# Kernel tuning notes

Measured on AMD Instinct MI355X. Metric: run time of the kernel, lower is better.

## Reference

```python
import jax, jax.numpy as jnp
import numpy as np

D = 1024   # embedding_dim
H = 16     # head_num
DH = D // H
STD = 0.02


def setup_inputs() -> dict:
    key = jax.random.key(0)
    ks = jax.random.split(key, 8)
    B, S = 16, 2048
    inp = {
        "hidden_states": jax.random.normal(ks[0], (B, S, D), dtype=jnp.float32),
        "attention_mask": jnp.zeros((B, 1, S), dtype=jnp.float32),
        # nn.Linear params, stored as [in, out] for direct matmul
        "Wq": jax.random.normal(ks[1], (D, D), dtype=jnp.float32) * STD,
        "bq": jnp.zeros((D,), dtype=jnp.float32),
        "Wqa": jax.random.normal(ks[2], (D, H), dtype=jnp.float32) * STD,
        "bqa": jnp.zeros((H,), dtype=jnp.float32),
        "Wk": jax.random.normal(ks[3], (D, D), dtype=jnp.float32) * STD,
        "bk": jnp.zeros((D,), dtype=jnp.float32),
        "Wka": jax.random.normal(ks[4], (D, H), dtype=jnp.float32) * STD,
        "bka": jnp.zeros((H,), dtype=jnp.float32),
        "Wt": jax.random.normal(ks[5], (D, D), dtype=jnp.float32) * STD,
        "bt": jnp.zeros((D,), dtype=jnp.float32),
    }
    return inp


def reference(hidden_states, attention_mask, Wq, bq, Wqa, bqa, Wk, bk, Wka, bka, Wt, bt):
    B, S, _ = hidden_states.shape
    scale = 1.0 / np.sqrt(DH).astype(np.float32)

    mixed_q = hidden_states @ Wq + bq          # [B,S,D]
    mixed_k = hidden_states @ Wk + bk          # [B,S,D]

    # per-head query pooling scores: [B,S,H] -> [B,H,S]
    q_score = jnp.transpose(mixed_q @ Wqa + bqa, (0, 2, 1)) * scale + attention_mask
    q_weight = jax.nn.softmax(q_score, axis=-1)                 # [B,H,S]

    q_layer = mixed_q.reshape(B, S, H, DH).transpose(0, 2, 1, 3)  # [B,H,S,dh]
    pooled_q = jnp.einsum('bhs,bhsd->bhd', q_weight, q_layer)     # [B,H,dh]
    pooled_q_flat = pooled_q.reshape(B, 1, D)                     # [B,1,D] (head-major)

    # elementwise modulate keys with pooled query (broadcast, no repeat)
    mixed_qk = mixed_k * pooled_q_flat                            # [B,S,D]

    qk_score = jnp.transpose(mixed_qk @ Wka + bka, (0, 2, 1)) * scale + attention_mask
    qk_weight = jax.nn.softmax(qk_score, axis=-1)                 # [B,H,S]

    k_layer = mixed_qk.reshape(B, S, H, DH).transpose(0, 2, 1, 3)  # [B,H,S,dh]
    pooled_k = jnp.einsum('bhs,bhsd->bhd', qk_weight, k_layer)     # [B,H,dh]

    weighted = pooled_k[:, :, None, :] * q_layer                   # [B,H,S,dh]
    weighted = weighted.transpose(0, 2, 1, 3).reshape(B, S, D)     # [B,S,D]

    return weighted @ Wt + bt + mixed_q
```

## Files before the change

kernel.cpp:

```cpp
#include <hip/hip_runtime.h>
#include <hip/hip_bf16.h>
#include <stdint.h>

#define D_ 1024
#define H_ 16
#define DH_ 64
#define S_ 2048
#define B_ 16
static constexpr float SCALE = 0.125f;

typedef __bf16 bf16_t;
typedef __bf16 bf16x8 __attribute__((ext_vector_type(8)));
typedef __bf16 bf16x4 __attribute__((ext_vector_type(4)));
typedef float  f32x4  __attribute__((ext_vector_type(4)));

__device__ __forceinline__ void llds16(const void* g, void* l) {
  __builtin_amdgcn_global_load_lds(
      (const __attribute__((address_space(1))) void*)g,
      (__attribute__((address_space(3))) void*)l, 16, 0, 0);
}

__global__ __launch_bounds__(256)
void f32_to_bf16(const float* __restrict__ src, bf16_t* __restrict__ dst) {
  size_t base = ((size_t)blockIdx.x * 256 + threadIdx.x) * 8;
  f32x4 a = *(const f32x4*)&src[base];
  f32x4 b = *(const f32x4*)&src[base + 4];
  bf16x8 o;
#pragma unroll
  for (int i = 0; i < 4; ++i) { o[i] = (bf16_t)a[i]; o[4 + i] = (bf16_t)b[i]; }
  *(bf16x8*)&dst[base] = o;
}

__global__ __launch_bounds__(256)
void transpose1024(const float* __restrict__ src, bf16_t* __restrict__ dst) {
  __shared__ bf16_t t[64][65];
  const int n0 = blockIdx.x * 64, k0 = blockIdx.y * 64;
  const int r = threadIdx.x >> 4, c4 = (threadIdx.x & 15) * 4;
#pragma unroll
  for (int p = 0; p < 4; ++p) {
    int row = p * 16 + r;
    f32x4 f = *(const f32x4*)&src[(size_t)(k0 + row) * 1024 + n0 + c4];
#pragma unroll
    for (int i = 0; i < 4; ++i) t[row][c4 + i] = (bf16_t)f[i];
  }
  __syncthreads();
#pragma unroll
  for (int p = 0; p < 4; ++p) {
    int row = p * 16 + r;
    bf16x4 v;
#pragma unroll
    for (int i = 0; i < 4; ++i) v[i] = t[c4 + i][row];
    *(bf16x4*)&dst[(size_t)(n0 + row) * 1024 + k0 + c4] = v;
  }
}

__global__ __launch_bounds__(256)
void transpose_small(const float* __restrict__ src, bf16_t* __restrict__ dst) {
  int k = blockIdx.x * 256 + threadIdx.x;
  if (k < 1024) {
#pragma unroll
    for (int h = 0; h < H_; ++h) dst[h * 1024 + k] = (bf16_t)src[k * H_ + h];
  }
}

__global__ __launch_bounds__(256)
void conv_misc(const float* bqa, const float* bka, const float* mask,
               bf16_t* obqa, bf16_t* obka, bf16_t* omask) {
  int i = blockIdx.x * 256 + threadIdx.x;
  const float* src; bf16_t* dst; int off;
  if      (i < 16)    { src = bqa;  dst = obqa;  off = i; }
  else if (i < 32)    { src = bka;  dst = obka;  off = i - 16; }
  else if (i < 32800) { src = mask; dst = omask; off = i - 32; }
  else return;
  dst[off] = (bf16_t)src[off];
}

template <int MODE>
__global__ __launch_bounds__(512, 1)
void gemm256(const bf16_t* __restrict__ A, const bf16_t* __restrict__ BT,
             const float* __restrict__ bias, void* __restrict__ Cout,
             const float* __restrict__ pscale, const bf16_t* __restrict__ resid) {
  constexpr int K = 1024;
  __shared__ __align__(16) bf16_t lds[2][2][256 * 64];
  const int tid = threadIdx.x;
  const int lane = tid & 63, wid = tid >> 6;
  const int wm = wid >> 2, wn = wid & 3;

  const int wgid = (blockIdx.x & 7) * 64 + (blockIdx.x >> 3);
  const int m0 = (wgid >> 2) * 256;
  const int n0 = (wgid & 3) * 256;

  const bf16_t* gA[4];
  const bf16_t* gB[4];
  int ldsOff[4];
#pragma unroll
  for (int i = 0; i < 4; ++i) {
    int c = i * 512 + tid;
    int r = c >> 3, j = c & 7;
    int col = ((j ^ (r & 7)) << 3);
    gA[i] = A  + (size_t)(m0 + r) * K + col;
    gB[i] = BT + (size_t)(n0 + r) * K + col;
    ldsOff[i] = c * 8;
  }

  f32x4 acc[8][4] = {};
  const int ar = lane & 15;
  const int kq = lane >> 4;

  bf16_t* curA = &lds[0][0][0]; bf16_t* curB = &lds[0][1][0];
  bf16_t* nxtA = &lds[1][0][0]; bf16_t* nxtB = &lds[1][1][0];

#pragma unroll
  for (int i = 0; i < 4; ++i) { llds16(gA[i], curA + ldsOff[i]); llds16(gB[i], curB + ldsOff[i]); }

  for (int t = 0; t < 16; ++t) {
    if (t < 15) {
      const int koff = (t + 1) * 64;
#pragma unroll
      for (int i = 0; i < 4; ++i) {
        llds16(gA[i] + koff, nxtA + ldsOff[i]);
        llds16(gB[i] + koff, nxtB + ldsOff[i]);
      }
      asm volatile("s_waitcnt vmcnt(8)" ::: "memory");
    } else {
      asm volatile("s_waitcnt vmcnt(0)" ::: "memory");
    }
    __builtin_amdgcn_s_barrier();

#pragma unroll
    for (int h = 0; h < 2; ++h) {
      bf16x8 af[8], bg[4];
#pragma unroll
      for (int m = 0; m < 8; ++m) {
        int r = wm * 128 + m * 16 + ar;
        af[m] = *(const bf16x8*)&curA[r * 64 + (((h * 4 + kq) ^ (r & 7)) << 3)];
      }
#pragma unroll
      for (int n = 0; n < 4; ++n) {
        int r = wn * 64 + n * 16 + ar;
        bg[n] = *(const bf16x8*)&curB[r * 64 + (((h * 4 + kq) ^ (r & 7)) << 3)];
      }
      __builtin_amdgcn_s_setprio(1);
#pragma unroll
      for (int m = 0; m < 8; ++m)
#pragma unroll
        for (int n = 0; n < 4; ++n)
          acc[m][n] = __builtin_amdgcn_mfma_f32_16x16x32_bf16(af[m], bg[n], acc[m][n], 0, 0, 0);
      __builtin_amdgcn_s_setprio(0);
    }
    __builtin_amdgcn_s_barrier();
    bf16_t* tA = curA; curA = nxtA; nxtA = tA;
    bf16_t* tB = curB; curB = nxtB; nxtB = tB;
  }

  float* st = (float*)(&lds[0][0][0]) + wid * (16 * 68);
  const int b = m0 / S_;
  const int erow = lane >> 2;
  const int ecol = (lane & 3) * 16;
  const int gcb = n0 + wn * 64;
  const int qrow = (lane >> 4) * 4;
  const int qcol = lane & 15;
  f32x4 bb[4], ps[4];
#pragma unroll
  for (int q = 0; q < 4; ++q) bb[q] = *(const f32x4*)&bias[gcb + ecol + q * 4];
  if (MODE == 1) {
#pragma unroll
    for (int q = 0; q < 4; ++q) ps[q] = *(const f32x4*)&pscale[b * D_ + gcb + ecol + q * 4];
  }
#pragma unroll
  for (int m = 0; m < 8; ++m) {
#pragma unroll
    for (int n = 0; n < 4; ++n)
#pragma unroll
      for (int j = 0; j < 4; ++j)
        st[(qrow + j) * 68 + n * 16 + qcol] = acc[m][n][j];
    asm volatile("s_waitcnt lgkmcnt(0)" ::: "memory");
    __builtin_amdgcn_sched_barrier(0);
    const int grow = m0 + wm * 128 + m * 16 + erow;
    f32x4 v[4];
#pragma unroll
    for (int q = 0; q < 4; ++q) v[q] = *(f32x4*)&st[erow * 68 + ecol + q * 4];
#pragma unroll
    for (int q = 0; q < 4; ++q)
#pragma unroll
      for (int i = 0; i < 4; ++i) v[q][i] += bb[q][i];
    if (MODE == 1) {
#pragma unroll
      for (int q = 0; q < 4; ++q)
#pragma unroll
        for (int i = 0; i < 4; ++i) v[q][i] *= ps[q][i];
    }
    if (MODE == 2) {
      bf16x8 r0 = *(const bf16x8*)&resid[(size_t)grow * D_ + gcb + ecol];
      bf16x8 r1 = *(const bf16x8*)&resid[(size_t)grow * D_ + gcb + ecol + 8];
#pragma unroll
      for (int i = 0; i < 4; ++i) { v[0][i] += (float)r0[i]; v[1][i] += (float)r0[4 + i]; }
#pragma unroll
      for (int i = 0; i < 4; ++i) { v[2][i] += (float)r1[i]; v[3][i] += (float)r1[4 + i]; }
      float* op = (float*)Cout + (size_t)grow * D_ + gcb + ecol;
#pragma unroll
      for (int q = 0; q < 4; ++q) *(f32x4*)&op[q * 4] = v[q];
    } else {
      bf16x8 o0, o1;
#pragma unroll
      for (int i = 0; i < 4; ++i) { o0[i] = (bf16_t)v[0][i]; o0[4 + i] = (bf16_t)v[1][i]; }
#pragma unroll
      for (int i = 0; i < 4; ++i) { o1[i] = (bf16_t)v[2][i]; o1[4 + i] = (bf16_t)v[3][i]; }
      bf16_t* op = (bf16_t*)Cout + (size_t)grow * D_ + gcb + ecol;
      *(bf16x8*)&op[0] = o0;
      *(bf16x8*)&op[8] = o1;
    }
  }
}

__global__ __launch_bounds__(256)
void score_kernel(const bf16_t* __restrict__ X, const bf16_t* __restrict__ WaT,
                  const bf16_t* __restrict__ ba, const bf16_t* __restrict__ mask,
                  float* __restrict__ scores) {
  const int lane = threadIdx.x & 63, wid = threadIdx.x >> 6;
  const int m0 = blockIdx.x * 64 + wid * 16;
  const int ar = lane & 15, ak = (lane >> 4) * 8;
  f32x4 acc = {};
  for (int k0 = 0; k0 < D_; k0 += 32) {
    bf16x8 a = *(const bf16x8*)&X[(size_t)(m0 + ar) * D_ + k0 + ak];
    bf16x8 b = *(const bf16x8*)&WaT[(size_t)ar * D_ + k0 + ak];
    acc = __builtin_amdgcn_mfma_f32_16x16x32_bf16(a, b, acc, 0, 0, 0);
  }
  const int h = lane & 15;
  const int srow = m0 + (lane >> 4) * 4;
  const int bb = srow / S_;
  const int s0 = srow - bb * S_;
  const float bah = (float)ba[h];
  f32x4 outv;
#pragma unroll
  for (int j = 0; j < 4; ++j)
    outv[j] = (acc[j] + bah) * SCALE + (float)mask[(size_t)bb * S_ + s0 + j];
  *(f32x4*)&scores[((size_t)(bb * H_ + h)) * S_ + s0] = outv;
}

__global__ __launch_bounds__(256)
void softmax_rows(const float* __restrict__ scores, float* __restrict__ wout) {
  __shared__ float rA[4], rB[4];
  const int tid = threadIdx.x, lane = tid & 63, wid = tid >> 6;
  const float* srow = scores + (size_t)blockIdx.x * S_;
  float* wrow = wout + (size_t)blockIdx.x * S_;
  f32x4 v0 = *(const f32x4*)&srow[tid * 4];
  f32x4 v1 = *(const f32x4*)&srow[1024 + tid * 4];
  float mx = fmaxf(fmaxf(fmaxf(v0[0], v0[1]), fmaxf(v0[2], v0[3])),
                   fmaxf(fmaxf(v1[0], v1[1]), fmaxf(v1[2], v1[3])));
#pragma unroll
  for (int o = 32; o; o >>= 1) mx = fmaxf(mx, __shfl_xor(mx, o));
  if (lane == 0) rA[wid] = mx;
  __syncthreads();
  mx = fmaxf(fmaxf(rA[0], rA[1]), fmaxf(rA[2], rA[3]));
  float sum = 0.f;
#pragma unroll
  for (int i = 0; i < 4; ++i) { v0[i] = __expf(v0[i] - mx); sum += v0[i]; }
#pragma unroll
  for (int i = 0; i < 4; ++i) { v1[i] = __expf(v1[i] - mx); sum += v1[i]; }
#pragma unroll
  for (int o = 32; o; o >>= 1) sum += __shfl_xor(sum, o);
  if (lane == 0) rB[wid] = sum;
  __syncthreads();
  sum = rB[0] + rB[1] + rB[2] + rB[3];
  const float inv = 1.0f / sum;
#pragma unroll
  for (int i = 0; i < 4; ++i) { v0[i] *= inv; v1[i] *= inv; }
  *(f32x4*)&wrow[tid * 4] = v0;
  *(f32x4*)&wrow[1024 + tid * 4] = v1;
}

__global__ __launch_bounds__(256)
void pool_partial(const bf16_t* __restrict__ X, const float* __restrict__ w,
                  float* __restrict__ partials) {
  __shared__ float sm[2][1024];
  const int tid = threadIdx.x;
  const int chunk = blockIdx.x, b = blockIdx.y;
  const int s0 = chunk * 32;
  const int dc = (tid & 127) * 8;
  const int sp = tid >> 7;
  const int h = dc >> 6;
  const float* wrow = w + ((size_t)b * H_ + h) * S_ + s0;
  const bf16_t* Xb = X + ((size_t)b * S_ + s0) * D_ + dc;
  float acc[8] = {};
  for (int s = sp; s < 32; s += 2) {
    bf16x8 xv = *(const bf16x8*)&Xb[(size_t)s * D_];
    float wt = wrow[s];
#pragma unroll
    for (int j = 0; j < 8; ++j) acc[j] += wt * (float)xv[j];
  }
#pragma unroll
  for (int j = 0; j < 8; ++j) sm[sp][dc + j] = acc[j];
  __syncthreads();
  const int d0 = tid * 4;
  f32x4 r;
#pragma unroll
  for (int j = 0; j < 4; ++j) r[j] = sm[0][d0 + j] + sm[1][d0 + j];
  *(f32x4*)&partials[((size_t)chunk * B_ + b) * D_ + d0] = r;
}

__global__ __launch_bounds__(256)
void pool_reduce(const float* __restrict__ partials, float* __restrict__ pooled) {
  const int idx = blockIdx.x * 256 + threadIdx.x;
  float s = 0.f;
#pragma unroll 8
  for (int c = 0; c < 64; ++c) s += partials[(size_t)c * (B_ * D_) + idx];
  pooled[idx] = s;
}

__global__ __launch_bounds__(256)
void weighted_kernel(const bf16_t* __restrict__ mq, const float* __restrict__ pk,
                     bf16_t* __restrict__ out) {
  size_t idx = ((size_t)blockIdx.x * 256 + threadIdx.x) * 8;
  int d0 = (int)(idx & (D_ - 1));
  int b = (int)(idx >> 21);
  bf16x8 v = *(const bf16x8*)&mq[idx];
  const float* pkb = pk + (size_t)b * D_ + d0;
  bf16x8 o;
#pragma unroll
  for (int i = 0; i < 8; ++i) o[i] = (bf16_t)((float)v[i] * pkb[i]);
  *(bf16x8*)&out[idx] = o;
}

extern "C" void kernel_launch(void* const* d_in, const int* in_sizes, int n_in,
                              void* d_out, int out_size, void* d_ws, size_t ws_size,
                              hipStream_t stream) {
  const float* hs   = (const float*)d_in[0];
  const float* mask = (const float*)d_in[1];
  const float* Wq   = (const float*)d_in[2];
  const float* bq   = (const float*)d_in[3];
  const float* Wqa  = (const float*)d_in[4];
  const float* bqa  = (const float*)d_in[5];
  const float* Wk   = (const float*)d_in[6];
  const float* bk   = (const float*)d_in[7];
  const float* Wka  = (const float*)d_in[8];
  const float* bka  = (const float*)d_in[9];
  const float* Wt   = (const float*)d_in[10];
  const float* bt   = (const float*)d_in[11];

  char* ws = (char*)d_ws;
  float*  pq    = (float*)(ws + (64u << 10));
  float*  pk    = (float*)(ws + (128u << 10));
  bf16_t* bqac  = (bf16_t*)(ws + (192u << 10));
  bf16_t* bkac  = (bf16_t*)(ws + (192u << 10) + 64);
  bf16_t* maskc = (bf16_t*)(ws + (256u << 10));
  bf16_t* WqaT  = (bf16_t*)(ws + (1u << 20));
  bf16_t* WkaT  = (bf16_t*)(ws + (1u << 20) + 32768);
  bf16_t* WqT   = (bf16_t*)(ws + (2u << 20));
  bf16_t* WkT   = (bf16_t*)(ws + (4u << 20));
  bf16_t* WtT   = (bf16_t*)(ws + (6u << 20));
  bf16_t* hsb   = (bf16_t*)(ws + (8u << 20));
  bf16_t* mq    = (bf16_t*)(ws + (8u << 20) + ((size_t)64 << 20));
  bf16_t* mqk   = (bf16_t*)(ws + (8u << 20) + ((size_t)128 << 20));
  bf16_t* wtd   = (bf16_t*)(ws + (8u << 20) + ((size_t)192 << 20));
  float* scores = (float*)(ws + (8u << 20) + ((size_t)256 << 20));
  float* wsm    = (float*)(ws + (8u << 20) + ((size_t)258 << 20));
  float* parts  = (float*)(ws + (8u << 20) + ((size_t)260 << 20));

  f32_to_bf16<<<16384, 256, 0, stream>>>(hs, hsb);
  conv_misc<<<129, 256, 0, stream>>>(bqa, bka, mask, bqac, bkac, maskc);
  transpose1024<<<dim3(16, 16), 256, 0, stream>>>(Wq, WqT);
  transpose1024<<<dim3(16, 16), 256, 0, stream>>>(Wk, WkT);
  transpose1024<<<dim3(16, 16), 256, 0, stream>>>(Wt, WtT);
  transpose_small<<<4, 256, 0, stream>>>(Wqa, WqaT);
  transpose_small<<<4, 256, 0, stream>>>(Wka, WkaT);

  gemm256<0><<<512, 512, 0, stream>>>(hsb, WqT, bq, mq, nullptr, nullptr);

  score_kernel<<<512, 256, 0, stream>>>(mq, WqaT, bqac, maskc, scores);
  softmax_rows<<<256, 256, 0, stream>>>(scores, wsm);
  pool_partial<<<dim3(64, 16), 256, 0, stream>>>(mq, wsm, parts);
  pool_reduce<<<64, 256, 0, stream>>>(parts, pq);

  gemm256<1><<<512, 512, 0, stream>>>(hsb, WkT, bk, mqk, pq, nullptr);

  score_kernel<<<512, 256, 0, stream>>>(mqk, WkaT, bkac, maskc, scores);
  softmax_rows<<<256, 256, 0, stream>>>(scores, wsm);
  pool_partial<<<dim3(64, 16), 256, 0, stream>>>(mqk, wsm, parts);
  pool_reduce<<<64, 256, 0, stream>>>(parts, pk);

  weighted_kernel<<<16384, 256, 0, stream>>>(mq, pk, wtd);

  gemm256<2><<<512, 512, 0, stream>>>(wtd, WtT, bt, d_out, nullptr, mq);
}
```

Measured before the change: 398.2 us.

## Replace 256-tile GEMM with 128-tile single-buffer GEMM and fuse weighting into A-load

Replaces the double-buffered 256x256 GEMM (512 threads, K-step 64, swizzled LDS) with a simpler 128x128 tile, 256-thread, K-step 32 kernel that has two workgroups per CU and no prefetch overlap. Folds the pooled-key weighting into the final GEMM's A-tile load, which removes the separate weighted kernel and its intermediate buffer. Merges the three weight transposes and the two small transposes into single launches. The GEMM loses its software pipelining and per-tile data reuse and synchronises twice per K-step, which may outweigh the fewer launches and the removed memory round trip.

```diff
diff --git a/kernel.cpp b/kernel.cpp
--- a/kernel.cpp
+++ b/kernel.cpp
@@ -32,8 +32,12 @@
 }
 
 __global__ __launch_bounds__(256)
-void transpose1024(const float* __restrict__ src, bf16_t* __restrict__ dst) {
+void transpose1024_all(const float* __restrict__ s0, const float* __restrict__ s1,
+                       const float* __restrict__ s2, bf16_t* __restrict__ d0,
+                       bf16_t* __restrict__ d1, bf16_t* __restrict__ d2) {
   __shared__ bf16_t t[64][65];
+  const float* src = (blockIdx.z == 0) ? s0 : (blockIdx.z == 1) ? s1 : s2;
+  bf16_t* dst      = (blockIdx.z == 0) ? d0 : (blockIdx.z == 1) ? d1 : d2;
   const int n0 = blockIdx.x * 64, k0 = blockIdx.y * 64;
   const int r = threadIdx.x >> 4, c4 = (threadIdx.x & 15) * 4;
 #pragma unroll
@@ -55,12 +59,14 @@
 }
 
 __global__ __launch_bounds__(256)
-void transpose_small(const float* __restrict__ src, bf16_t* __restrict__ dst) {
-  int k = blockIdx.x * 256 + threadIdx.x;
-  if (k < 1024) {
-#pragma unroll
-    for (int h = 0; h < H_; ++h) dst[h * 1024 + k] = (bf16_t)src[k * H_ + h];
-  }
+void transpose_small_all(const float* __restrict__ sa, const float* __restrict__ sb,
+                         bf16_t* __restrict__ da, bf16_t* __restrict__ db) {
+  int g = blockIdx.x * 256 + threadIdx.x;
+  const float* src = (g < 1024) ? sa : sb;
+  bf16_t* dst      = (g < 1024) ? da : db;
+  int k = g & 1023;
+#pragma unroll
+  for (int h = 0; h < H_; ++h) dst[h * 1024 + k] = (bf16_t)src[k * H_ + h];
 }
 
 __global__ __launch_bounds__(256)
@@ -76,88 +82,85 @@
 }
 
 template <int MODE>
-__global__ __launch_bounds__(512, 1)
-void gemm256(const bf16_t* __restrict__ A, const bf16_t* __restrict__ BT,
+__global__ __launch_bounds__(256, 2)
+void gemm_bt(const bf16_t* __restrict__ A, const bf16_t* __restrict__ BT,
              const float* __restrict__ bias, void* __restrict__ Cout,
-             const float* __restrict__ pscale, const bf16_t* __restrict__ resid) {
-  constexpr int K = 1024;
-  __shared__ __align__(16) bf16_t lds[2][2][256 * 64];
+             const float* __restrict__ pscale, const bf16_t* __restrict__ resid,
+             const float* __restrict__ pkA) {
+  constexpr int K = 1024, N = 1024;
+  __shared__ __align__(16) bf16_t lA[128 * 32];
+  __shared__ __align__(16) bf16_t lB[128 * 32];
+  __shared__ __align__(16) float est[4][16 * 68];
   const int tid = threadIdx.x;
   const int lane = tid & 63, wid = tid >> 6;
-  const int wm = wid >> 2, wn = wid & 3;
-
-  const int wgid = (blockIdx.x & 7) * 64 + (blockIdx.x >> 3);
-  const int m0 = (wgid >> 2) * 256;
-  const int n0 = (wgid & 3) * 256;
-
-  const bf16_t* gA[4];
-  const bf16_t* gB[4];
-  int ldsOff[4];
-#pragma unroll
-  for (int i = 0; i < 4; ++i) {
-    int c = i * 512 + tid;
-    int r = c >> 3, j = c & 7;
-    int col = ((j ^ (r & 7)) << 3);
-    gA[i] = A  + (size_t)(m0 + r) * K + col;
-    gB[i] = BT + (size_t)(n0 + r) * K + col;
-    ldsOff[i] = c * 8;
-  }
-
-  f32x4 acc[8][4] = {};
+  const int wr = wid >> 1, wc = wid & 1;
+
+  const int wgid = (blockIdx.x & 7) * 256 + (blockIdx.x >> 3);
+  const int m0 = (wgid >> 3) * 128;
+  const int n0 = (wgid & 7) * 128;
+  const int b = m0 / S_;
+
   const int ar = lane & 15;
   const int kq = lane >> 4;
 
-  bf16_t* curA = &lds[0][0][0]; bf16_t* curB = &lds[0][1][0];
-  bf16_t* nxtA = &lds[1][0][0]; bf16_t* nxtB = &lds[1][1][0];
-
-#pragma unroll
-  for (int i = 0; i < 4; ++i) { llds16(gA[i], curA + ldsOff[i]); llds16(gB[i], curB + ldsOff[i]); }
-
-  for (int t = 0; t < 16; ++t) {
-    if (t < 15) {
-      const int koff = (t + 1) * 64;
-#pragma unroll
-      for (int i = 0; i < 4; ++i) {
-        llds16(gA[i] + koff, nxtA + ldsOff[i]);
-        llds16(gB[i] + koff, nxtB + ldsOff[i]);
+  int rowc[2], colc[2], dstoff[2];
+#pragma unroll
+  for (int j = 0; j < 2; ++j) {
+    int c = j * 256 + tid;
+    int row = c >> 2, s = c & 3;
+    rowc[j] = row;
+    colc[j] = (((s - (row >> 1)) & 3) << 3);
+    dstoff[j] = c * 8;
+  }
+
+  f32x4 acc[4][4] = {};
+
+  for (int k0 = 0; k0 < K; k0 += 32) {
+#pragma unroll
+    for (int j = 0; j < 2; ++j) {
+      const bf16_t* gb = BT + (size_t)(n0 + rowc[j]) * K + k0 + colc[j];
+      llds16(gb, lB + dstoff[j]);
+      if (MODE == 2) {
+        bf16x8 v = *(const bf16x8*)(A + (size_t)(m0 + rowc[j]) * K + k0 + colc[j]);
+        const float* pkp = pkA + b * D_ + k0 + colc[j];
+        f32x4 p0 = *(const f32x4*)pkp;
+        f32x4 p1 = *(const f32x4*)(pkp + 4);
+        bf16x8 o;
+#pragma unroll
+        for (int i = 0; i < 4; ++i) {
+          o[i]     = (bf16_t)((float)v[i] * p0[i]);
+          o[4 + i] = (bf16_t)((float)v[4 + i] * p1[i]);
+        }
+        *(bf16x8*)&lA[dstoff[j]] = o;
+      } else {
+        const bf16_t* ga = A + (size_t)(m0 + rowc[j]) * K + k0 + colc[j];
+        llds16(ga, lA + dstoff[j]);
       }
-      asm volatile("s_waitcnt vmcnt(8)" ::: "memory");
-    } else {
-      asm volatile("s_waitcnt vmcnt(0)" ::: "memory");
-    }
-    __builtin_amdgcn_s_barrier();
-
-#pragma unroll
-    for (int h = 0; h < 2; ++h) {
-      bf16x8 af[8], bg[4];
-#pragma unroll
-      for (int m = 0; m < 8; ++m) {
-        int r = wm * 128 + m * 16 + ar;
-        af[m] = *(const bf16x8*)&curA[r * 64 + (((h * 4 + kq) ^ (r & 7)) << 3)];
-      }
-#pragma unroll
-      for (int n = 0; n < 4; ++n) {
-        int r = wn * 64 + n * 16 + ar;
-        bg[n] = *(const bf16x8*)&curB[r * 64 + (((h * 4 + kq) ^ (r & 7)) << 3)];
-      }
-      __builtin_amdgcn_s_setprio(1);
-#pragma unroll
-      for (int m = 0; m < 8; ++m)
-#pragma unroll
-        for (int n = 0; n < 4; ++n)
-          acc[m][n] = __builtin_amdgcn_mfma_f32_16x16x32_bf16(af[m], bg[n], acc[m][n], 0, 0, 0);
-      __builtin_amdgcn_s_setprio(0);
-    }
-    __builtin_amdgcn_s_barrier();
-    bf16_t* tA = curA; curA = nxtA; nxtA = tA;
-    bf16_t* tB = curB; curB = nxtB; nxtB = tB;
-  }
-
-  float* st = (float*)(&lds[0][0][0]) + wid * (16 * 68);
-  const int b = m0 / S_;
+    }
+    __syncthreads();
+    bf16x8 af[4], bg[4];
+#pragma unroll
+    for (int m = 0; m < 4; ++m) {
+      int r = wr * 64 + m * 16 + ar;
+      af[m] = *(const bf16x8*)&lA[r * 32 + (((kq + (r >> 1)) & 3) << 3)];
+    }
+#pragma unroll
+    for (int n = 0; n < 4; ++n) {
+      int r = wc * 64 + n * 16 + ar;
+      bg[n] = *(const bf16x8*)&lB[r * 32 + (((kq + (r >> 1)) & 3) << 3)];
+    }
+#pragma unroll
+    for (int m = 0; m < 4; ++m)
+#pragma unroll
+      for (int n = 0; n < 4; ++n)
+        acc[m][n] = __builtin_amdgcn_mfma_f32_16x16x32_bf16(af[m], bg[n], acc[m][n], 0, 0, 0);
+    __syncthreads();
+  }
+
+  float* st = est[wid];
   const int erow = lane >> 2;
   const int ecol = (lane & 3) * 16;
-  const int gcb = n0 + wn * 64;
+  const int gcb = n0 + wc * 64;
   const int qrow = (lane >> 4) * 4;
   const int qcol = lane & 15;
   f32x4 bb[4], ps[4];
@@ -168,7 +171,7 @@
     for (int q = 0; q < 4; ++q) ps[q] = *(const f32x4*)&pscale[b * D_ + gcb + ecol + q * 4];
   }
 #pragma unroll
-  for (int m = 0; m < 8; ++m) {
+  for (int m = 0; m < 4; ++m) {
 #pragma unroll
     for (int n = 0; n < 4; ++n)
 #pragma unroll
@@ -176,7 +179,7 @@
         st[(qrow + j) * 68 + n * 16 + qcol] = acc[m][n][j];
     asm volatile("s_waitcnt lgkmcnt(0)" ::: "memory");
     __builtin_amdgcn_sched_barrier(0);
-    const int grow = m0 + wm * 128 + m * 16 + erow;
+    const int grow = m0 + wr * 64 + m * 16 + erow;
     f32x4 v[4];
 #pragma unroll
     for (int q = 0; q < 4; ++q) v[q] = *(f32x4*)&st[erow * 68 + ecol + q * 4];
@@ -191,13 +194,13 @@
         for (int i = 0; i < 4; ++i) v[q][i] *= ps[q][i];
     }
     if (MODE == 2) {
-      bf16x8 r0 = *(const bf16x8*)&resid[(size_t)grow * D_ + gcb + ecol];
-      bf16x8 r1 = *(const bf16x8*)&resid[(size_t)grow * D_ + gcb + ecol + 8];
+      bf16x8 r0 = *(const bf16x8*)&resid[(size_t)grow * N + gcb + ecol];
+      bf16x8 r1 = *(const bf16x8*)&resid[(size_t)grow * N + gcb + ecol + 8];
 #pragma unroll
       for (int i = 0; i < 4; ++i) { v[0][i] += (float)r0[i]; v[1][i] += (float)r0[4 + i]; }
 #pragma unroll
       for (int i = 0; i < 4; ++i) { v[2][i] += (float)r1[i]; v[3][i] += (float)r1[4 + i]; }
-      float* op = (float*)Cout + (size_t)grow * D_ + gcb + ecol;
+      float* op = (float*)Cout + (size_t)grow * N + gcb + ecol;
 #pragma unroll
       for (int q = 0; q < 4; ++q) *(f32x4*)&op[q * 4] = v[q];
     } else {
@@ -206,7 +209,7 @@
       for (int i = 0; i < 4; ++i) { o0[i] = (bf16_t)v[0][i]; o0[4 + i] = (bf16_t)v[1][i]; }
 #pragma unroll
       for (int i = 0; i < 4; ++i) { o1[i] = (bf16_t)v[2][i]; o1[4 + i] = (bf16_t)v[3][i]; }
-      bf16_t* op = (bf16_t*)Cout + (size_t)grow * D_ + gcb + ecol;
+      bf16_t* op = (bf16_t*)Cout + (size_t)grow * N + gcb + ecol;
       *(bf16x8*)&op[0] = o0;
       *(bf16x8*)&op[8] = o1;
     }
@@ -308,20 +311,6 @@
   pooled[idx] = s;
 }
 
-__global__ __launch_bounds__(256)
-void weighted_kernel(const bf16_t* __restrict__ mq, const float* __restrict__ pk,
-                     bf16_t* __restrict__ out) {
-  size_t idx = ((size_t)blockIdx.x * 256 + threadIdx.x) * 8;
-  int d0 = (int)(idx & (D_ - 1));
-  int b = (int)(idx >> 21);
-  bf16x8 v = *(const bf16x8*)&mq[idx];
-  const float* pkb = pk + (size_t)b * D_ + d0;
-  bf16x8 o;
-#pragma unroll
-  for (int i = 0; i < 8; ++i) o[i] = (bf16_t)((float)v[i] * pkb[i]);
-  *(bf16x8*)&out[idx] = o;
-}
-
 extern "C" void kernel_launch(void* const* d_in, const int* in_sizes, int n_in,
                               void* d_out, int out_size, void* d_ws, size_t ws_size,
                               hipStream_t stream) {
@@ -352,34 +341,28 @@
   bf16_t* hsb   = (bf16_t*)(ws + (8u << 20));
   bf16_t* mq    = (bf16_t*)(ws + (8u << 20) + ((size_t)64 << 20));
   bf16_t* mqk   = (bf16_t*)(ws + (8u << 20) + ((size_t)128 << 20));
-  bf16_t* wtd   = (bf16_t*)(ws + (8u << 20) + ((size_t)192 << 20));
-  float* scores = (float*)(ws + (8u << 20) + ((size_t)256 << 20));
-  float* wsm    = (float*)(ws + (8u << 20) + ((size_t)258 << 20));
-  float* parts  = (float*)(ws + (8u << 20) + ((size_t)260 << 20));
+  float* scores = (float*)(ws + (8u << 20) + ((size_t)192 << 20));
+  float* wsm    = (float*)(ws + (8u << 20) + ((size_t)194 << 20));
+  float* parts  = (float*)(ws + (8u << 20) + ((size_t)196 << 20));
 
   f32_to_bf16<<<16384, 256, 0, stream>>>(hs, hsb);
   conv_misc<<<129, 256, 0, stream>>>(bqa, bka, mask, bqac, bkac, maskc);
-  transpose1024<<<dim3(16, 16), 256, 0, stream>>>(Wq, WqT);
-  transpose1024<<<dim3(16, 16), 256, 0, stream>>>(Wk, WkT);
-  transpose1024<<<dim3(16, 16), 256, 0, stream>>>(Wt, WtT);
-  transpose_small<<<4, 256, 0, stream>>>(Wqa, WqaT);
-  transpose_small<<<4, 256, 0, stream>>>(Wka, WkaT);
-
-  gemm256<0><<<512, 512, 0, stream>>>(hsb, WqT, bq, mq, nullptr, nullptr);
+  transpose1024_all<<<dim3(16, 16, 3), 256, 0, stream>>>(Wq, Wk, Wt, WqT, WkT, WtT);
+  transpose_small_all<<<8, 256, 0, stream>>>(Wqa, Wka, WqaT, WkaT);
+
+  gemm_bt<0><<<2048, 256, 0, stream>>>(hsb, WqT, bq, mq, nullptr, nullptr, nullptr);
 
   score_kernel<<<512, 256, 0, stream>>>(mq, WqaT, bqac, maskc, scores);
   softmax_rows<<<256, 256, 0, stream>>>(scores, wsm);
   pool_partial<<<dim3(64, 16), 256, 0, stream>>>(mq, wsm, parts);
   pool_reduce<<<64, 256, 0, stream>>>(parts, pq);
 
-  gemm256<1><<<512, 512, 0, stream>>>(hsb, WkT, bk, mqk, pq, nullptr);
+  gemm_bt<1><<<2048, 256, 0, stream>>>(hsb, WkT, bk, mqk, pq, nullptr, nullptr);
 
   score_kernel<<<512, 256, 0, stream>>>(mqk, WkaT, bkac, maskc, scores);
   softmax_rows<<<256, 256, 0, stream>>>(scores, wsm);
   pool_partial<<<dim3(64, 16), 256, 0, stream>>>(mqk, wsm, parts);
   pool_reduce<<<64, 256, 0, stream>>>(parts, pk);
 
-  weighted_kernel<<<16384, 256, 0, stream>>>(mq, pk, wtd);
-
-  gemm256<2><<<512, 512, 0, stream>>>(wtd, WtT, bt, d_out, nullptr, mq);
-}
+  gemm_bt<2><<<2048, 256, 0, stream>>>(mq, WtT, bt, d_out, nullptr, mq, pk);
+}
```

Result: no change. 394.0 us (-1.0%).
